# Performance work log

Measured on AMD Instinct MI355X. Metric: run time of the kernel, lower is better.

## Reference

```python
import jax, jax.numpy as jnp
import numpy as np

N, E = 40000, 640000
DIN, HID, H = 512, 128, 4
C = HID  # per-head channels; H*C == 512 == DIN
BN_EPS = 1e-5


def setup_inputs() -> dict:
    key = jax.random.key(0)
    ks = jax.random.split(key, 32)
    sc = 0.05
    d = {}
    d["x"] = jax.random.normal(ks[0], (N, DIN), jnp.float32)
    d["edge_index"] = jax.random.randint(ks[1], (2, E), 0, N)
    i = 2
    for l in (1, 2, 3):
        d[f"W{l}"] = jax.random.normal(ks[i], (DIN, H * C), jnp.float32) * sc; i += 1
        d[f"as{l}"] = jax.random.normal(ks[i], (H, C), jnp.float32) * sc; i += 1
        d[f"ad{l}"] = jax.random.normal(ks[i], (H, C), jnp.float32) * sc; i += 1
        d[f"b{l}"] = jnp.zeros((H * C,), jnp.float32)
        d[f"g{l}"] = jnp.ones((H * C,), jnp.float32)
        d[f"be{l}"] = jnp.zeros((H * C,), jnp.float32)
    d["Wg1"] = jax.random.normal(ks[i], (H * C, HID), jnp.float32) * sc; i += 1
    d["bg1"] = jnp.zeros((HID,), jnp.float32)
    d["Wg2"] = jax.random.normal(ks[i], (HID, 1), jnp.float32) * sc; i += 1
    d["bg2"] = jnp.zeros((1,), jnp.float32)
    d["Wf1"] = jax.random.normal(ks[i], (H * C, HID), jnp.float32) * sc; i += 1
    d["bf1"] = jnp.zeros((HID,), jnp.float32)
    d["Wf2"] = jax.random.normal(ks[i], (HID, HID), jnp.float32) * sc; i += 1
    d["bf2"] = jnp.zeros((HID,), jnp.float32)
    d["Wp"] = jax.random.normal(ks[i], (HID + H * C, HID), jnp.float32) * sc; i += 1
    d["bp"] = jnp.zeros((HID,), jnp.float32)
    return d


def _gat(x, src, dst, W, a_s, a_d, b):
    # PyG GATConv (concat=True, negative_slope=0.2, self-loops already in src/dst)
    n = x.shape[0]
    h = (x @ W).reshape(n, H, C)                      # [N,H,C]
    es = jnp.einsum('nhc,hc->nh', h, a_s)             # alpha_src per node
    ed = jnp.einsum('nhc,hc->nh', h, a_d)             # alpha_dst per node
    e = jax.nn.leaky_relu(es[src] + ed[dst], 0.2)     # [Etot,H]
    m = jax.ops.segment_max(e, dst, num_segments=n)   # softmax over incoming edges
    ex = jnp.exp(e - m[dst])
    s = jax.ops.segment_sum(ex, dst, num_segments=n)
    w = ex / (s[dst] + 1e-16)                         # [Etot,H]
    out = jax.ops.segment_sum(w[:, :, None] * h[src], dst, num_segments=n)
    return out.reshape(n, H * C) + b


def _bn(x, g, b):
    mu = x.mean(0)
    var = x.var(0)
    return (x - mu) * jax.lax.rsqrt(var + BN_EPS) * g + b


def reference(x, edge_index,
              W1, as1, ad1, b1, g1, be1,
              W2, as2, ad2, b2, g2, be2,
              W3, as3, ad3, b3, g3, be3,
              Wg1, bg1, Wg2, bg2, Wf1, bf1, Wf2, bf2, Wp, bp):
    n = x.shape[0]
    loops = jnp.arange(n)
    src = jnp.concatenate([edge_index[0], loops])
    dst = jnp.concatenate([edge_index[1], loops])

    h = jax.nn.leaky_relu(_bn(_gat(x, src, dst, W1, as1, ad1, b1), g1, be1), 0.2)
    h_res = h
    h = jax.nn.leaky_relu(_bn(_gat(h, src, dst, W2, as2, ad2, b2), g2, be2), 0.2) + h_res
    h_res = h
    h = jax.nn.leaky_relu(_bn(_gat(h, src, dst, W3, as3, ad3, b3), g3, be3), 0.2) + h_res

    attn_scores = (jnp.tanh(h @ Wg1 + bg1) @ Wg2 + bg2)[:, 0]   # [N]
    attn_w = jax.nn.softmax(attn_scores)                        # softmax over all nodes
    feat = jax.nn.relu(h @ Wf1 + bf1) @ Wf2 + bf2               # [N,HID]
    gated = (attn_w[:, None] * feat).sum(0)                     # [HID]
    global_pooled = h.mean(0, keepdims=True)                    # batch=None -> one graph
    combined = jnp.concatenate([gated[None, :], global_pooled], axis=-1)  # [1,640]
    out = (combined @ Wp + bp)[0]                               # [HID]
    return out, attn_scores
```

## Files before the change

### kernel.cpp

```cpp
#include <hip/hip_runtime.h>
#include <math.h>

#define N_NODES 40000
#define M_PAD   40064
#define N_EDGES 640000
#define ETOT    (N_EDGES + N_NODES)
#define DINC    512
#define NHEAD   4
#define CHD     128
#define BN_EPS  1e-5f

typedef __attribute__((ext_vector_type(8))) short bf16x8;
typedef __attribute__((ext_vector_type(4))) float f32x4;

static __device__ __forceinline__ float lrelu(float x) { return x > 0.f ? x : 0.2f * x; }

static __device__ __forceinline__ unsigned short f2b(float f) {
    union { float f; unsigned int u; } v; v.f = f;
    unsigned int r = (v.u + 0x7fff + ((v.u >> 16) & 1)) >> 16;
    return (unsigned short)r;
}
static __device__ __forceinline__ float b2f(unsigned short b) {
    union { unsigned int u; float f; } v; v.u = ((unsigned int)b) << 16;
    return v.f;
}
static __device__ __forceinline__ float lo16(unsigned int u) {
    union { unsigned int u; float f; } v; v.u = u << 16; return v.f;
}
static __device__ __forceinline__ float hi16(unsigned int u) {
    union { unsigned int u; float f; } v; v.u = u & 0xffff0000u; return v.f;
}

static __device__ __forceinline__ void fma8(float* acc, uint4 hv, float wgt) {
    acc[0] += wgt * lo16(hv.x); acc[1] += wgt * hi16(hv.x);
    acc[2] += wgt * lo16(hv.y); acc[3] += wgt * hi16(hv.y);
    acc[4] += wgt * lo16(hv.z); acc[5] += wgt * hi16(hv.z);
    acc[6] += wgt * lo16(hv.w); acc[7] += wgt * hi16(hv.w);
}

#define GLDS16(g, l) __builtin_amdgcn_global_load_lds( \
    (__attribute__((address_space(1))) void*)(g),      \
    (__attribute__((address_space(3))) void*)(l), 16, 0, 0)

#define CVTX_BLK 10000
__global__ __launch_bounds__(256) void k_prep(const float4* __restrict__ xin,
                                              uint4* __restrict__ xb,
                                              uint4* __restrict__ curb,
                                              uint4* __restrict__ cnt4) {
    int bid = blockIdx.x;
    int tid = threadIdx.x;
    if (bid < CVTX_BLK) {
        size_t i = (size_t)bid * 256 + tid;
        float4 a = xin[i * 2], b = xin[i * 2 + 1];
        uint4 o;
        o.x = (unsigned)f2b(a.x) | ((unsigned)f2b(a.y) << 16);
        o.y = (unsigned)f2b(a.z) | ((unsigned)f2b(a.w) << 16);
        o.z = (unsigned)f2b(b.x) | ((unsigned)f2b(b.y) << 16);
        o.w = (unsigned)f2b(b.z) | ((unsigned)f2b(b.w) << 16);
        xb[i] = o;
    } else if (bid < CVTX_BLK + 16) {
        int i = (bid - CVTX_BLK) * 256 + tid;
        xb[(size_t)N_NODES * DINC / 8 + i] = make_uint4(0, 0, 0, 0);
    } else if (bid < CVTX_BLK + 32) {
        int i = (bid - CVTX_BLK - 16) * 256 + tid;
        curb[(size_t)N_NODES * DINC / 8 + i] = make_uint4(0, 0, 0, 0);
    } else {
        int i = (bid - CVTX_BLK - 32) * 256 + tid;
        if (i < N_NODES / 4) cnt4[i] = make_uint4(0, 0, 0, 0);
    }
}

__global__ __launch_bounds__(256) void k_cvtw_all(const float* __restrict__ W1, unsigned short* __restrict__ T1,
                                                  const float* __restrict__ W2, unsigned short* __restrict__ T2,
                                                  const float* __restrict__ W3, unsigned short* __restrict__ T3,
                                                  const float* __restrict__ Wg1, const float* __restrict__ Wf1,
                                                  unsigned short* __restrict__ Wct) {
    int idx = blockIdx.x * 256 + threadIdx.x;
    const float* W; unsigned short* T; int Nn;
    if (idx < 262144)            { W = W1; T = T1; Nn = 512; }
    else if (idx < 524288)       { W = W2; T = T2; Nn = 512; idx -= 262144; }
    else if (idx < 786432)       { W = W3; T = T3; Nn = 512; idx -= 524288; }
    else if (idx < 851968)       { W = Wg1; T = Wct; Nn = 128; idx -= 786432; }
    else                         { W = Wf1; T = Wct + 65536; Nn = 128; idx -= 851968; }
    int k = idx / Nn, n = idx % Nn;
    T[(size_t)n * 512 + k] = f2b(W[idx]);
}

__global__ void k_degree(const int* __restrict__ ei, int* __restrict__ cnt) {
    int e = blockIdx.x * 256 + threadIdx.x;
    if (e < ETOT) {
        int dst = (e < N_EDGES) ? ei[N_EDGES + e] : (e - N_EDGES);
        atomicAdd(&cnt[dst], 1);
    }
}

__global__ __launch_bounds__(64) void k_scan1(const int* __restrict__ deg, int* __restrict__ bsum) {
    int lane = threadIdx.x;
    int v = deg[blockIdx.x * 64 + lane];
#pragma unroll
    for (int off = 32; off; off >>= 1) v += __shfl_xor(v, off);
    if (lane == 0) bsum[blockIdx.x] = v;
}

__global__ __launch_bounds__(64) void k_scan23(const int* __restrict__ deg, const int* __restrict__ bsum,
                                               int* __restrict__ rowptr, int* __restrict__ cnt) {
    int b = blockIdx.x, lane = threadIdx.x;
    int pre = 0;
    for (int i = lane; i < b; i += 64) pre += bsum[i];
#pragma unroll
    for (int off = 32; off; off >>= 1) pre += __shfl_xor(pre, off);
    int i = b * 64 + lane;
    int v = deg[i];
    int inc = v;
#pragma unroll
    for (int off = 1; off < 64; off <<= 1) {
        int t = __shfl_up(inc, off);
        if (lane >= off) inc += t;
    }
    rowptr[i] = pre + inc - v;
    cnt[i] = 0;
    if (b == 624 && lane == 63) rowptr[N_NODES] = ETOT;
}

__global__ void k_fill(const int* __restrict__ ei, const int* __restrict__ rowptr,
                       int* __restrict__ cnt, int* __restrict__ csr_src) {
    int e = blockIdx.x * 256 + threadIdx.x;
    if (e < ETOT) {
        int src, dst;
        if (e < N_EDGES) { src = ei[e]; dst = ei[N_EDGES + e]; }
        else             { src = e - N_EDGES; dst = src; }
        int pos = rowptr[dst] + atomicAdd(&cnt[dst], 1);
        csr_src[pos] = src;
    }
}

template<int CBF16, int EPI>
__global__ __launch_bounds__(256) void k_gemm_mfma(const unsigned short* __restrict__ A,
                                                   const unsigned short* __restrict__ Bt,
                                                   void* __restrict__ Cout,
                                                   int Nn, int K, int nbn,
                                                   const float* __restrict__ p1,
                                                   const float* __restrict__ p2,
                                                   float* __restrict__ p3,
                                                   float* __restrict__ p4,
                                                   const float* __restrict__ p5,
                                                   const float* __restrict__ p6) {
    __shared__ alignas(16) unsigned short As[128 * 64];
    __shared__ alignas(16) unsigned short Bs[128 * 64];
    const int tid  = threadIdx.x;
    const int wv   = tid >> 6;
    const int lane = tid & 63;
    const int bm = (blockIdx.x / nbn) * 128;
    const int bn = (blockIdx.x % nbn) * 128;
    const int wm = (wv >> 1) * 64;
    const int wn = (wv & 1) * 64;

    const int srow = lane >> 3;
    const int scol = (((lane & 7) ^ srow) * 8);
    const size_t a_base = (size_t)(bm + wv * 32 + srow) * K + scol;
    const size_t b_base = (size_t)(bn + wv * 32 + srow) * K + scol;

    f32x4 acc[4][4] = {};

    for (int k0 = 0; k0 < K; k0 += 64) {
#pragma unroll
        for (int q = 0; q < 4; ++q)
            GLDS16(A + a_base + (size_t)q * 8 * K + k0, &As[(wv * 32 + q * 8) * 64]);
#pragma unroll
        for (int q = 0; q < 4; ++q)
            GLDS16(Bt + b_base + (size_t)q * 8 * K + k0, &Bs[(wv * 32 + q * 8) * 64]);
        __syncthreads();

        const int r0 = lane & 15;
#pragma unroll
        for (int ks = 0; ks < 2; ++ks) {
            const int c = ks * 4 + (lane >> 4);
            bf16x8 af[4], bfr[4];
#pragma unroll
            for (int i = 0; i < 4; ++i) {
                int row = wm + i * 16 + r0;
                af[i] = *(const bf16x8*)&As[row * 64 + ((c ^ (row & 7)) * 8)];
            }
#pragma unroll
            for (int j = 0; j < 4; ++j) {
                int row = wn + j * 16 + r0;
                bfr[j] = *(const bf16x8*)&Bs[row * 64 + ((c ^ (row & 7)) * 8)];
            }
#pragma unroll
            for (int i = 0; i < 4; ++i)
#pragma unroll
                for (int j = 0; j < 4; ++j)
                    acc[i][j] = __builtin_amdgcn_mfma_f32_16x16x32_bf16(af[i], bfr[j], acc[i][j], 0, 0, 0);
        }
        __syncthreads();
    }

    const int crow0 = bm + wm + (lane >> 4) * 4;
    const int ccol  = bn + wn + (lane & 15);

    if (EPI != 2) {
#pragma unroll
        for (int i = 0; i < 4; ++i)
#pragma unroll
            for (int j = 0; j < 4; ++j)
#pragma unroll
                for (int r = 0; r < 4; ++r) {
                    size_t off = (size_t)(crow0 + i * 16 + r) * Nn + ccol + j * 16;
                    if (CBF16) ((unsigned short*)Cout)[off] = f2b(acc[i][j][r]);
                    else       ((float*)Cout)[off] = acc[i][j][r];
                }
    }

    if (EPI == 1) {
        const int head = bn >> 7;
        float asv[4], adv[4];
#pragma unroll
        for (int j = 0; j < 4; ++j) {
            int cc = head * CHD + wn + j * 16 + (lane & 15);
            asv[j] = p1[cc];
            adv[j] = p2[cc];
        }
        float* sE = (float*)As;
        sE[tid] = 0.f;
        __syncthreads();
#pragma unroll
        for (int i = 0; i < 4; ++i)
#pragma unroll
            for (int r = 0; r < 4; ++r) {
                float e = acc[i][0][r] * asv[0] + acc[i][1][r] * asv[1]
                        + acc[i][2][r] * asv[2] + acc[i][3][r] * asv[3];
                float d = acc[i][0][r] * adv[0] + acc[i][1][r] * adv[1]
                        + acc[i][2][r] * adv[2] + acc[i][3][r] * adv[3];
#pragma unroll
                for (int off = 8; off; off >>= 1) {
                    e += __shfl_xor(e, off);
                    d += __shfl_xor(d, off);
                }
                if ((lane & 15) == 0) {
                    int rloc = wm + i * 16 + (lane >> 4) * 4 + r;
                    atomicAdd(&sE[rloc], e);
                    atomicAdd(&sE[128 + rloc], d);
                }
            }
        __syncthreads();
        if (tid < 128) {
            p3[(size_t)(bm + tid) * NHEAD + head] = sE[tid];
            p4[(size_t)(bm + tid) * NHEAD + head] = sE[128 + tid];
        }
    }

    if (EPI == 2) {
        if (bn == 0) {
            float wgv[4], bgv[4];
#pragma unroll
            for (int j = 0; j < 4; ++j) {
                int cc = wn + j * 16 + (lane & 15);
                bgv[j] = p1[cc];
                wgv[j] = p2[cc];
            }
            float* sE = (float*)As;
            sE[tid] = 0.f;
            __syncthreads();
#pragma unroll
            for (int i = 0; i < 4; ++i)
#pragma unroll
                for (int r = 0; r < 4; ++r) {
                    float e = tanhf(acc[i][0][r] + bgv[0]) * wgv[0]
                            + tanhf(acc[i][1][r] + bgv[1]) * wgv[1]
                            + tanhf(acc[i][2][r] + bgv[2]) * wgv[2]
                            + tanhf(acc[i][3][r] + bgv[3]) * wgv[3];
#pragma unroll
                    for (int off = 8; off; off >>= 1) e += __shfl_xor(e, off);
                    if ((lane & 15) == 0)
                        atomicAdd(&sE[wm + i * 16 + (lane >> 4) * 4 + r], e);
                }
            __syncthreads();
            if (tid < 128) p3[bm + tid] = sE[tid] + p5[0];
        } else {
#pragma unroll
            for (int j = 0; j < 4; ++j) {
                int colF = wn + j * 16 + (lane & 15);
                float bv = p6[colF];
#pragma unroll
                for (int i = 0; i < 4; ++i)
#pragma unroll
                    for (int r = 0; r < 4; ++r)
                        p4[(size_t)(crow0 + i * 16 + r) * 128 + colF] =
                            fmaxf(acc[i][j][r] + bv, 0.f);
            }
        }
    }
}

__global__ __launch_bounds__(256) void k_wts(const float4* __restrict__ es4,
                                             const float4* __restrict__ ed4,
                                             const int* __restrict__ rowptr,
                                             const int* __restrict__ csr_src,
                                             float4* __restrict__ wbuf4,
                                             float4* __restrict__ inv4,
                                             float* __restrict__ stats) {
    if (blockIdx.x == 0)
        for (int q = threadIdx.x; q < DINC * 2; q += 256) stats[q] = 0.f;
    int n = blockIdx.x * 4 + (threadIdx.x >> 6);
    int lane = threadIdx.x & 63;
    int start = rowptr[n], end = rowptr[n + 1];
    float4 edn = ed4[n];
    float4 mx = make_float4(-1e30f, -1e30f, -1e30f, -1e30f);
    for (int j0 = start; j0 < end; j0 += 64) {
        int j = j0 + lane;
        if (j < end) {
            int s = csr_src[j];
            float4 e = es4[s];
            mx.x = fmaxf(mx.x, lrelu(e.x + edn.x));
            mx.y = fmaxf(mx.y, lrelu(e.y + edn.y));
            mx.z = fmaxf(mx.z, lrelu(e.z + edn.z));
            mx.w = fmaxf(mx.w, lrelu(e.w + edn.w));
        }
    }
#pragma unroll
    for (int off = 32; off; off >>= 1) {
        mx.x = fmaxf(mx.x, __shfl_xor(mx.x, off));
        mx.y = fmaxf(mx.y, __shfl_xor(mx.y, off));
        mx.z = fmaxf(mx.z, __shfl_xor(mx.z, off));
        mx.w = fmaxf(mx.w, __shfl_xor(mx.w, off));
    }
    float4 sum = make_float4(0.f, 0.f, 0.f, 0.f);
    for (int j0 = start; j0 < end; j0 += 64) {
        int j = j0 + lane;
        if (j < end) {
            int s = csr_src[j];
            float4 e = es4[s];
            float4 ex;
            ex.x = __expf(lrelu(e.x + edn.x) - mx.x);
            ex.y = __expf(lrelu(e.y + edn.y) - mx.y);
            ex.z = __expf(lrelu(e.z + edn.z) - mx.z);
            ex.w = __expf(lrelu(e.w + edn.w) - mx.w);
            wbuf4[j] = ex;
            sum.x += ex.x; sum.y += ex.y; sum.z += ex.z; sum.w += ex.w;
        }
    }
#pragma unroll
    for (int off = 32; off; off >>= 1) {
        sum.x += __shfl_xor(sum.x, off);
        sum.y += __shfl_xor(sum.y, off);
        sum.z += __shfl_xor(sum.z, off);
        sum.w += __shfl_xor(sum.w, off);
    }
    if (lane == 0) {
        float4 iv;
        iv.x = 1.f / (sum.x + 1e-16f);
        iv.y = 1.f / (sum.y + 1e-16f);
        iv.z = 1.f / (sum.z + 1e-16f);
        iv.w = 1.f / (sum.w + 1e-16f);
        inv4[n] = iv;
    }
}

__global__ __launch_bounds__(256) void k_agg(const unsigned short* __restrict__ hb,
                                             const int* __restrict__ rowptr,
                                             const int* __restrict__ csr_src,
                                             const float* __restrict__ wbuf,
                                             const float* __restrict__ invp,
                                             unsigned short* __restrict__ aggb) {
    __shared__ float part[4][512];
    const int n = blockIdx.x;
    const int tid = threadIdx.x;
    const int grp = tid >> 6;
    const int lane = tid & 63;
    const int head = lane >> 4;
    const int start = rowptr[n], end = rowptr[n + 1];

    float acc[8] = {};
    int j = start + grp;
    int s_n = 0; float w_n = 0.f;
    if (j < end) { s_n = csr_src[j]; w_n = wbuf[j * 4 + head]; }
    while (j < end) {
        int s = s_n; float wgt = w_n;
        int j2 = j + 4;
        if (j2 < end) { s_n = csr_src[j2]; w_n = wbuf[j2 * 4 + head]; }
        uint4 hv = *(const uint4*)&hb[(size_t)s * DINC + lane * 8];
        fma8(acc, hv, wgt);
        j = j2;
    }
    *(float4*)&part[grp][lane * 8]     = make_float4(acc[0], acc[1], acc[2], acc[3]);
    *(float4*)&part[grp][lane * 8 + 4] = make_float4(acc[4], acc[5], acc[6], acc[7]);
    __syncthreads();
    const int c = tid * 2;
    float v0 = part[0][c] + part[1][c] + part[2][c] + part[3][c];
    float v1 = part[0][c + 1] + part[1][c + 1] + part[2][c + 1] + part[3][c + 1];
    float iv = invp[(n << 2) + (c >> 7)];
    v0 *= iv; v1 *= iv;
    unsigned int o = (unsigned)f2b(v0) | ((unsigned)f2b(v1) << 16);
    *(unsigned int*)&aggb[(size_t)n * DINC + c] = o;
}

__global__ __launch_bounds__(256) void k_bn_stats(const unsigned short* __restrict__ aggb,
                                                  float* __restrict__ stats) {
    int tid = threadIdx.x;
    int row0 = blockIdx.x * 64;
    int c0 = tid * 2;
    float s0 = 0, q0 = 0, s1 = 0, q1 = 0;
    for (int r = row0; r < row0 + 64; ++r) {
        unsigned int hv = *(const unsigned int*)&aggb[(size_t)r * DINC + c0];
        float v0 = lo16(hv), v1 = hi16(hv);
        s0 += v0; q0 += v0 * v0;
        s1 += v1; q1 += v1 * v1;
    }
    atomicAdd(&stats[c0], s0);
    atomicAdd(&stats[c0 + 1], s1);
    atomicAdd(&stats[DINC + c0], q0);
    atomicAdd(&stats[DINC + c0 + 1], q1);
}

__global__ __launch_bounds__(256) void k_bn_act(const unsigned short* __restrict__ aggb,
                                                const float* __restrict__ stats,
                                                const float* __restrict__ g,
                                                const float* __restrict__ be,
                                                unsigned short* __restrict__ curb,
                                                int res) {
    size_t idx = (size_t)blockIdx.x * 256 + threadIdx.x;
    int c8 = ((int)(idx & 63)) * 8;
    uint4 v = *(const uint4*)&aggb[idx * 8];
    float xv[8] = { lo16(v.x), hi16(v.x), lo16(v.y), hi16(v.y),
                    lo16(v.z), hi16(v.z), lo16(v.w), hi16(v.w) };
#pragma unroll
    for (int q = 0; q < 8; ++q) {
        int c = c8 + q;
        float mu = stats[c] * (1.f / N_NODES);
        float var = stats[DINC + c] * (1.f / N_NODES) - mu * mu;
        float A = g[c] * rsqrtf(var + BN_EPS);
        float B = be[c] - mu * A;
        xv[q] = lrelu(xv[q] * A + B);
    }
    if (res) {
        uint4 r = *(const uint4*)&curb[idx * 8];
        xv[0] += lo16(r.x); xv[1] += hi16(r.x);
        xv[2] += lo16(r.y); xv[3] += hi16(r.y);
        xv[4] += lo16(r.z); xv[5] += hi16(r.z);
        xv[6] += lo16(r.w); xv[7] += hi16(r.w);
    }
    uint4 o;
    o.x = (unsigned)f2b(xv[0]) | ((unsigned)f2b(xv[1]) << 16);
    o.y = (unsigned)f2b(xv[2]) | ((unsigned)f2b(xv[3]) << 16);
    o.z = (unsigned)f2b(xv[4]) | ((unsigned)f2b(xv[5]) << 16);
    o.w = (unsigned)f2b(xv[6]) | ((unsigned)f2b(xv[7]) << 16);
    *(uint4*)&curb[idx * 8] = o;
}

__global__ __launch_bounds__(1024) void k_softmax(const float* __restrict__ scores, float* __restrict__ sm,
                                                  float* __restrict__ vbuf, float* __restrict__ pooled) {
    __shared__ float red[16];
    int tid = threadIdx.x, lane = tid & 63, wv = tid >> 6;
    if (tid < 128) vbuf[tid] = 0.f;
    if (tid < DINC) pooled[tid] = 0.f;
    float m = -1e30f;
    for (int i = tid; i < N_NODES; i += 1024) m = fmaxf(m, scores[i]);
#pragma unroll
    for (int off = 32; off; off >>= 1) m = fmaxf(m, __shfl_xor(m, off));
    if (lane == 0) red[wv] = m;
    __syncthreads();
    float mall = red[0];
    for (int i = 1; i < 16; ++i) mall = fmaxf(mall, red[i]);
    __syncthreads();
    float s = 0.f;
    for (int i = tid; i < N_NODES; i += 1024) s += expf(scores[i] - mall);
#pragma unroll
    for (int off = 32; off; off >>= 1) s += __shfl_xor(s, off);
    if (lane == 0) red[wv] = s;
    __syncthreads();
    if (tid == 0) {
        float tot = 0.f;
        for (int i = 0; i < 16; ++i) tot += red[i];
        sm[0] = mall; sm[1] = tot;
    }
}

__global__ __launch_bounds__(640) void k_vpool(const float* __restrict__ Fb,
                                               const unsigned short* __restrict__ hb,
                                               const float* __restrict__ scores,
                                               const float* __restrict__ sm,
                                               float* __restrict__ v,
                                               float* __restrict__ pooled) {
    int tid = threadIdx.x;
    int row0 = blockIdx.x * 64;
    float mall = sm[0];
    float invS = 1.f / sm[1];
    if (tid < 128) {
        float acc = 0.f;
        for (int r = row0; r < row0 + 64; ++r) {
            float w = expf(scores[r] - mall) * invS;
            acc += w * Fb[(size_t)r * 128 + tid];
        }
        atomicAdd(&v[tid], acc);
    } else {
        int c = tid - 128;
        float acc = 0.f;
        for (int r = row0; r < row0 + 64; ++r) acc += b2f(hb[(size_t)r * DINC + c]);
        atomicAdd(&pooled[c], acc * (1.f / N_NODES));
    }
}

__global__ __launch_bounds__(128) void k_final(const float* __restrict__ v,
                                               const float* __restrict__ pooled,
                                               const float* __restrict__ Wf2,
                                               const float* __restrict__ bf2,
                                               const float* __restrict__ Wp,
                                               const float* __restrict__ bp,
                                               float* __restrict__ out) {
    __shared__ float sg[128];
    int o = threadIdx.x;
    float g = bf2[o];
    for (int k = 0; k < 128; ++k) g += v[k] * Wf2[k * 128 + o];
    sg[o] = g;
    __syncthreads();
    float acc = bp[o];
    for (int c = 0; c < 128; ++c) acc += sg[c] * Wp[c * 128 + o];
    for (int j = 0; j < 512; ++j) acc += pooled[j] * Wp[(128 + j) * 128 + o];
    out[o] = acc;
}

extern "C" void kernel_launch(void* const* d_in, const int* in_sizes, int n_in,
                              void* d_out, int out_size, void* d_ws, size_t ws_size,
                              hipStream_t stream) {
    const float* x  = (const float*)d_in[0];
    const int*   ei = (const int*)d_in[1];
    const float* Wg1 = (const float*)d_in[20];
    const float* bg1 = (const float*)d_in[21];
    const float* Wg2 = (const float*)d_in[22];
    const float* bg2 = (const float*)d_in[23];
    const float* Wf1 = (const float*)d_in[24];
    const float* bf1 = (const float*)d_in[25];
    const float* Wf2 = (const float*)d_in[26];
    const float* bf2 = (const float*)d_in[27];
    const float* Wp  = (const float*)d_in[28];
    const float* bp  = (const float*)d_in[29];
    float* out = (float*)d_out;

    char* base = (char*)d_ws;
    size_t off = 0;
    auto take = [&](size_t nbytes) -> char* {
        char* p = base + off;
        off += (nbytes + 255) & ~(size_t)255;
        return p;
    };
    unsigned short* hb   = (unsigned short*)take((size_t)M_PAD * DINC * 2);
    unsigned short* curb = (unsigned short*)take((size_t)M_PAD * DINC * 2);
    unsigned short* xb   = (unsigned short*)take((size_t)M_PAD * DINC * 2);
    unsigned short* aggb = (unsigned short*)take((size_t)M_PAD * DINC * 2);
    float* Fb    = (float*)take((size_t)M_PAD * 128 * 4);
    float* es    = (float*)take((size_t)M_PAD * NHEAD * 4);
    float* ed    = (float*)take((size_t)M_PAD * NHEAD * 4);
    float* wbuf  = (float*)take((size_t)ETOT * NHEAD * 4);
    float* invp  = (float*)take((size_t)N_NODES * NHEAD * 4);
    int*   rowptr= (int*)take((size_t)(N_NODES + 1) * 4);
    int*   cnt   = (int*)take((size_t)N_NODES * 4);
    int*   csr   = (int*)take((size_t)ETOT * 4);
    int*   bsum  = (int*)take(625 * 4);
    float* stats = (float*)take(DINC * 2 * 4);
    float* sm    = (float*)take(2 * 4);
    float* vbuf  = (float*)take(128 * 4);
    float* pooled= (float*)take(DINC * 4);
    unsigned short* Wt1  = (unsigned short*)take((size_t)DINC * DINC * 2);
    unsigned short* Wt2  = (unsigned short*)take((size_t)DINC * DINC * 2);
    unsigned short* Wt3  = (unsigned short*)take((size_t)DINC * DINC * 2);
    unsigned short* Wct  = (unsigned short*)take((size_t)256 * DINC * 2);

    k_prep<<<CVTX_BLK + 32 + 40, 256, 0, stream>>>((const float4*)x, (uint4*)xb,
                                                   (uint4*)curb, (uint4*)cnt);
    k_cvtw_all<<<3584, 256, 0, stream>>>((const float*)d_in[2], Wt1,
                                         (const float*)d_in[8], Wt2,
                                         (const float*)d_in[14], Wt3,
                                         Wg1, Wf1, Wct);
    k_degree<<<(ETOT + 255) / 256, 256, 0, stream>>>(ei, cnt);
    k_scan1<<<625, 64, 0, stream>>>(cnt, bsum);
    k_scan23<<<625, 64, 0, stream>>>(cnt, bsum, rowptr, cnt);
    k_fill<<<(ETOT + 255) / 256, 256, 0, stream>>>(ei, rowptr, cnt, csr);

    const unsigned short* Wts[3] = {Wt1, Wt2, Wt3};
    const unsigned short* in = xb;
    for (int l = 0; l < 3; ++l) {
        const float* as_ = (const float*)d_in[2 + l * 6 + 1];
        const float* ad_ = (const float*)d_in[2 + l * 6 + 2];
        const float* g   = (const float*)d_in[2 + l * 6 + 4];
        const float* be  = (const float*)d_in[2 + l * 6 + 5];

        k_gemm_mfma<1, 1><<<(M_PAD / 128) * (DINC / 128), 256, 0, stream>>>(
            in, Wts[l], hb, DINC, DINC, DINC / 128, as_, ad_, es, ed, nullptr, nullptr);
        k_wts<<<N_NODES / 4, 256, 0, stream>>>((const float4*)es, (const float4*)ed, rowptr, csr,
                                               (float4*)wbuf, (float4*)invp, stats);
        k_agg<<<N_NODES, 256, 0, stream>>>(hb, rowptr, csr, wbuf, invp, aggb);
        k_bn_stats<<<N_NODES / 64, 256, 0, stream>>>(aggb, stats);
        k_bn_act<<<(N_NODES * (DINC / 8)) / 256, 256, 0, stream>>>(aggb, stats, g, be, curb, l > 0 ? 1 : 0);
        in = curb;
    }

    float* scores = out + 128;
    k_gemm_mfma<0, 2><<<(M_PAD / 128) * 2, 256, 0, stream>>>(
        curb, Wct, nullptr, 256, DINC, 2, bg1, Wg2, scores, Fb, bg2, bf1);

    k_softmax<<<1, 1024, 0, stream>>>(scores, sm, vbuf, pooled);
    k_vpool<<<N_NODES / 64, 640, 0, stream>>>(Fb, curb, scores, sm, vbuf, pooled);
    k_final<<<1, 128, 0, stream>>>(vbuf, pooled, Wf2, bf2, Wp, bp, out);
}
```

Baseline: 891.6 us.

## Store edge softmax weights as bf16 and vectorize softmax/pooling reductions

The per-edge attention numerators are now packed as bf16 (8 bytes per edge instead of 16), which halves the write traffic in k_wts and the read traffic in k_agg. The aggregation kernel unpacks the value for its head. Separately, the global softmax loop reads scores as float4 and uses __expf, and k_vpool loads two bf16 channels per thread with a 384-thread block. The main risk is a small precision loss in the attention weights. The float4 cast of scores assumes the pointer (out+128) is 16-byte aligned.

Measured after the change: 879.9 us. About the same (-1.3%).

```diff
diff --git a/kernel.cpp b/kernel.cpp
--- a/kernel.cpp
+++ b/kernel.cpp
@@ -296,7 +296,7 @@
                                              const float4* __restrict__ ed4,
                                              const int* __restrict__ rowptr,
                                              const int* __restrict__ csr_src,
-                                             float4* __restrict__ wbuf4,
+                                             uint2* __restrict__ wbuf2,
                                              float4* __restrict__ inv4,
                                              float* __restrict__ stats) {
     if (blockIdx.x == 0)
@@ -335,7 +335,8 @@
             ex.y = __expf(lrelu(e.y + edn.y) - mx.y);
             ex.z = __expf(lrelu(e.z + edn.z) - mx.z);
             ex.w = __expf(lrelu(e.w + edn.w) - mx.w);
-            wbuf4[j] = ex;
+            wbuf2[j] = make_uint2((unsigned)f2b(ex.x) | ((unsigned)f2b(ex.y) << 16),
+                                  (unsigned)f2b(ex.z) | ((unsigned)f2b(ex.w) << 16));
             sum.x += ex.x; sum.y += ex.y; sum.z += ex.z; sum.w += ex.w;
         }
     }
@@ -359,7 +360,7 @@
 __global__ __launch_bounds__(256) void k_agg(const unsigned short* __restrict__ hb,
                                              const int* __restrict__ rowptr,
                                              const int* __restrict__ csr_src,
-                                             const float* __restrict__ wbuf,
+                                             const unsigned* __restrict__ wbufu,
                                              const float* __restrict__ invp,
                                              unsigned short* __restrict__ aggb) {
     __shared__ float part[4][512];
@@ -368,16 +369,18 @@
     const int grp = tid >> 6;
     const int lane = tid & 63;
     const int head = lane >> 4;
+    const int hh = head >> 1;
     const int start = rowptr[n], end = rowptr[n + 1];
 
     float acc[8] = {};
     int j = start + grp;
-    int s_n = 0; float w_n = 0.f;
-    if (j < end) { s_n = csr_src[j]; w_n = wbuf[j * 4 + head]; }
+    int s_n = 0; unsigned wu_n = 0;
+    if (j < end) { s_n = csr_src[j]; wu_n = wbufu[j * 2 + hh]; }
     while (j < end) {
-        int s = s_n; float wgt = w_n;
+        int s = s_n; unsigned wu = wu_n;
         int j2 = j + 4;
-        if (j2 < end) { s_n = csr_src[j2]; w_n = wbuf[j2 * 4 + head]; }
+        if (j2 < end) { s_n = csr_src[j2]; wu_n = wbufu[j2 * 2 + hh]; }
+        float wgt = (head & 1) ? hi16(wu) : lo16(wu);
         uint4 hv = *(const uint4*)&hb[(size_t)s * DINC + lane * 8];
         fma8(acc, hv, wgt);
         j = j2;
@@ -447,14 +450,19 @@
     *(uint4*)&curb[idx * 8] = o;
 }
 
-__global__ __launch_bounds__(1024) void k_softmax(const float* __restrict__ scores, float* __restrict__ sm,
+__global__ __launch_bounds__(1024) void k_softmax(const float4* __restrict__ scores4,
+                                                  const float* __restrict__ scores,
+                                                  float* __restrict__ sm,
                                                   float* __restrict__ vbuf, float* __restrict__ pooled) {
     __shared__ float red[16];
     int tid = threadIdx.x, lane = tid & 63, wv = tid >> 6;
     if (tid < 128) vbuf[tid] = 0.f;
     if (tid < DINC) pooled[tid] = 0.f;
     float m = -1e30f;
-    for (int i = tid; i < N_NODES; i += 1024) m = fmaxf(m, scores[i]);
+    for (int i = tid; i < N_NODES / 4; i += 1024) {
+        float4 s4 = scores4[i];
+        m = fmaxf(fmaxf(fmaxf(m, s4.x), fmaxf(s4.y, s4.z)), s4.w);
+    }
 #pragma unroll
     for (int off = 32; off; off >>= 1) m = fmaxf(m, __shfl_xor(m, off));
     if (lane == 0) red[wv] = m;
@@ -463,7 +471,10 @@
     for (int i = 1; i < 16; ++i) mall = fmaxf(mall, red[i]);
     __syncthreads();
     float s = 0.f;
-    for (int i = tid; i < N_NODES; i += 1024) s += expf(scores[i] - mall);
+    for (int i = tid; i < N_NODES / 4; i += 1024) {
+        float4 s4 = scores4[i];
+        s += __expf(s4.x - mall) + __expf(s4.y - mall) + __expf(s4.z - mall) + __expf(s4.w - mall);
+    }
 #pragma unroll
     for (int off = 32; off; off >>= 1) s += __shfl_xor(s, off);
     if (lane == 0) red[wv] = s;
@@ -475,7 +486,7 @@
     }
 }
 
-__global__ __launch_bounds__(640) void k_vpool(const float* __restrict__ Fb,
+__global__ __launch_bounds__(384) void k_vpool(const float* __restrict__ Fb,
                                                const unsigned short* __restrict__ hb,
                                                const float* __restrict__ scores,
                                                const float* __restrict__ sm,
@@ -488,15 +499,19 @@
     if (tid < 128) {
         float acc = 0.f;
         for (int r = row0; r < row0 + 64; ++r) {
-            float w = expf(scores[r] - mall) * invS;
+            float w = __expf(scores[r] - mall) * invS;
             acc += w * Fb[(size_t)r * 128 + tid];
         }
         atomicAdd(&v[tid], acc);
     } else {
-        int c = tid - 128;
-        float acc = 0.f;
-        for (int r = row0; r < row0 + 64; ++r) acc += b2f(hb[(size_t)r * DINC + c]);
-        atomicAdd(&pooled[c], acc * (1.f / N_NODES));
+        int c = (tid - 128) * 2;
+        float a0 = 0.f, a1 = 0.f;
+        for (int r = row0; r < row0 + 64; ++r) {
+            unsigned int hv = *(const unsigned int*)&hb[(size_t)r * DINC + c];
+            a0 += lo16(hv); a1 += hi16(hv);
+        }
+        atomicAdd(&pooled[c], a0 * (1.f / N_NODES));
+        atomicAdd(&pooled[c + 1], a1 * (1.f / N_NODES));
     }
 }
 
@@ -550,7 +565,7 @@
     float* Fb    = (float*)take((size_t)M_PAD * 128 * 4);
     float* es    = (float*)take((size_t)M_PAD * NHEAD * 4);
     float* ed    = (float*)take((size_t)M_PAD * NHEAD * 4);
-    float* wbuf  = (float*)take((size_t)ETOT * NHEAD * 4);
+    uint2* wbuf  = (uint2*)take((size_t)ETOT * 8);
     float* invp  = (float*)take((size_t)N_NODES * NHEAD * 4);
     int*   rowptr= (int*)take((size_t)(N_NODES + 1) * 4);
     int*   cnt   = (int*)take((size_t)N_NODES * 4);
@@ -587,8 +602,8 @@
         k_gemm_mfma<1, 1><<<(M_PAD / 128) * (DINC / 128), 256, 0, stream>>>(
             in, Wts[l], hb, DINC, DINC, DINC / 128, as_, ad_, es, ed, nullptr, nullptr);
         k_wts<<<N_NODES / 4, 256, 0, stream>>>((const float4*)es, (const float4*)ed, rowptr, csr,
-                                               (float4*)wbuf, (float4*)invp, stats);
-        k_agg<<<N_NODES, 256, 0, stream>>>(hb, rowptr, csr, wbuf, invp, aggb);
+                                               wbuf, (float4*)invp, stats);
+        k_agg<<<N_NODES, 256, 0, stream>>>(hb, rowptr, csr, (const unsigned*)wbuf, invp, aggb);
         k_bn_stats<<<N_NODES / 64, 256, 0, stream>>>(aggb, stats);
         k_bn_act<<<(N_NODES * (DINC / 8)) / 256, 256, 0, stream>>>(aggb, stats, g, be, curb, l > 0 ? 1 : 0);
         in = curb;
@@ -598,7 +613,7 @@
     k_gemm_mfma<0, 2><<<(M_PAD / 128) * 2, 256, 0, stream>>>(
         curb, Wct, nullptr, 256, DINC, 2, bg1, Wg2, scores, Fb, bg2, bf1);
 
-    k_softmax<<<1, 1024, 0, stream>>>(scores, sm, vbuf, pooled);
-    k_vpool<<<N_NODES / 64, 640, 0, stream>>>(Fb, curb, scores, sm, vbuf, pooled);
+    k_softmax<<<1, 1024, 0, stream>>>((const float4*)scores, scores, sm, vbuf, pooled);
+    k_vpool<<<N_NODES / 64, 384, 0, stream>>>(Fb, curb, scores, sm, vbuf, pooled);
     k_final<<<1, 128, 0, stream>>>(vbuf, pooled, Wf2, bf2, Wp, bp, out);
 }
```
